# Optimization experiments

Measured on AMD Instinct MI355X. Metric: run time of the kernel, lower is better.

## Reference

```python
import jax, jax.numpy as jnp
import numpy as np

B, S, D = 8, 2048, 768
H, HD = 12, 64  # num_heads, head_dim = embed_dim // num_heads
EPS = 1e-6


def setup_inputs() -> dict:
    key = jax.random.key(0)
    ks = jax.random.split(key, 9)
    sc = 0.02
    return {
        "x": jax.random.normal(ks[0], (B, S, D), jnp.float32),
        "Wq": jax.random.normal(ks[1], (H, D, HD), jnp.float32) * sc,
        "bq": jax.random.normal(ks[2], (H, HD), jnp.float32) * sc,
        "Wk": jax.random.normal(ks[3], (H, D, HD), jnp.float32) * sc,
        "bk": jax.random.normal(ks[4], (H, HD), jnp.float32) * sc,
        "Wv": jax.random.normal(ks[5], (H, D, HD), jnp.float32) * sc,
        "bv": jax.random.normal(ks[6], (H, HD), jnp.float32) * sc,
        "Wp": jax.random.normal(ks[7], (D, D), jnp.float32) * sc,
        "bp": jax.random.normal(ks[8], (D,), jnp.float32) * sc,
    }


def reference(x, Wq, bq, Wk, bk, Wv, bv, Wp, bp):
    # Batched per-head projections (the torch loop over heads, vectorized).
    Q = jnp.einsum("bsd,hde->bhse", x, Wq) + bq[:, None, :]  # [B,H,S,HD]
    K = jnp.einsum("bsd,hde->bhse", x, Wk) + bk[:, None, :]
    V = jnp.einsum("bsd,hde->bhse", x, Wv) + bv[:, None, :]
    scale = jnp.sqrt(jnp.float32(HD)) + EPS  # intended 1/sqrt(head_dim) scaling
    scores = jnp.einsum("bhse,bhte->bhst", Q, K) / scale  # [B,H,S,S]
    attn = jax.nn.softmax(scores, axis=-1)
    ctx = jnp.einsum("bhst,bhte->bhse", attn, V)  # [B,H,S,HD]
    # concat heads along last dim (head i -> slice i*HD:(i+1)*HD), then project
    ctx = jnp.transpose(ctx, (0, 2, 1, 3)).reshape(B, S, H * HD)
    return ctx @ Wp + bp
```

## Files before the change

kernel.cpp:

```cpp
#include <hip/hip_runtime.h>
#include <hip/hip_bf16.h>
#include <stdint.h>

#define B_  8
#define S_  2048
#define D_  768
#define H_  12
#define HD_ 64
#define BH_ (B_*H_)
#define M_  (B_*S_)

typedef __bf16 bf16;
typedef __bf16 bf16x8 __attribute__((ext_vector_type(8)));
typedef __bf16 bf16x4 __attribute__((ext_vector_type(4)));
typedef short  short4v __attribute__((ext_vector_type(4)));
typedef float  f32x4  __attribute__((ext_vector_type(4)));

#define QSCALE2 0.18033685756901243f

#if __has_builtin(__builtin_amdgcn_exp2f)
#define EXP2(x) __builtin_amdgcn_exp2f(x)
#else
#define EXP2(x) exp2f(x)
#endif

#define LDS_BARRIER() asm volatile("s_waitcnt lgkmcnt(0)\n\ts_barrier" ::: "memory")

#define GLD16(gptr, lptr) __builtin_amdgcn_global_load_lds( \
    (const __attribute__((address_space(1))) uint32_t*)(gptr), \
    (__attribute__((address_space(3))) uint32_t*)(lptr), 16, 0, 0)

#if __has_builtin(__builtin_amdgcn_mfma_f32_16x16x16bf16_1k)
static __device__ inline f32x4 mfma16(bf16x4 a, bf16x4 b, f32x4 c) {
  return __builtin_amdgcn_mfma_f32_16x16x16bf16_1k(
      __builtin_bit_cast(short4v, a), __builtin_bit_cast(short4v, b), c, 0, 0, 0);
}
#else
static __device__ inline f32x4 mfma16(bf16x4 a, bf16x4 b, f32x4 c) {
  bf16 z = (bf16)0.f;
  bf16x8 a8 = {a[0], a[1], a[2], a[3], z, z, z, z};
  bf16x8 b8 = {b[0], b[1], b[2], b[3], z, z, z, z};
  return __builtin_amdgcn_mfma_f32_16x16x32_bf16(a8, b8, c, 0, 0, 0);
}
#endif

__global__ __launch_bounds__(256) void f2b(const float* __restrict__ src,
                                           bf16* __restrict__ dst, int n) {
  int i = (blockIdx.x * 256 + threadIdx.x) * 8;
  if (i >= n) return;
  float4 a = *(const float4*)(src + i);
  float4 b = *(const float4*)(src + i + 4);
  bf16 o[8] = {(bf16)a.x, (bf16)a.y, (bf16)a.z, (bf16)a.w,
               (bf16)b.x, (bf16)b.y, (bf16)b.z, (bf16)b.w};
  *(uint4*)(dst + i) = *(const uint4*)o;
}

__global__ __launch_bounds__(256) void transpose64_f2b(const float* __restrict__ src,
                                                       bf16* __restrict__ dst,
                                                       int R, int C) {
  __shared__ bf16 t[64][72];
  int mat = blockIdx.z;
  const float* s = src + (size_t)mat * R * C;
  bf16* d = dst + (size_t)mat * C * R;
  int r0 = blockIdx.x * 64, c0 = blockIdx.y * 64;
  int tid = threadIdx.x;
  #pragma unroll
  for (int it = 0; it < 4; ++it) {
    int i = (tid >> 4) + it * 16;
    int j = (tid & 15) * 4;
    float4 v = *(const float4*)(s + (size_t)(r0 + i) * C + c0 + j);
    t[j + 0][i] = (bf16)v.x; t[j + 1][i] = (bf16)v.y;
    t[j + 2][i] = (bf16)v.z; t[j + 3][i] = (bf16)v.w;
  }
  __syncthreads();
  #pragma unroll
  for (int it = 0; it < 4; ++it) {
    int i = (tid >> 4) + it * 16;
    int j = (tid & 15) * 4;
    bf16* p = d + (size_t)(c0 + i) * R + r0 + j;
    p[0] = t[i][j]; p[1] = t[i][j + 1]; p[2] = t[i][j + 2]; p[3] = t[i][j + 3];
  }
}

__global__ __launch_bounds__(256) void prep_w(
    const float* __restrict__ Wq, const float* __restrict__ Wk,
    const float* __restrict__ Wv, const float* __restrict__ bq,
    const float* __restrict__ bk, const float* __restrict__ bv,
    bf16* __restrict__ Wt, float* __restrict__ ball)
{
  int z = blockIdx.z;
  int tid = threadIdx.x;
  if (z == 36) {
    int i = blockIdx.x * 256 + tid;
    if (i < 2304) {
      float v = (i < 768) ? bq[i] : (i < 1536 ? bk[i - 768] : bv[i - 1536]);
      ball[i] = v;
    }
    return;
  }
  __shared__ bf16 t[64][72];
  int w = z / 12, h = z % 12;
  const float* s = (w == 0 ? Wq : (w == 1 ? Wk : Wv)) + (size_t)h * 768 * 64;
  bf16* d = Wt + (size_t)z * 64 * 768;
  int r0 = blockIdx.x * 64;
  #pragma unroll
  for (int it = 0; it < 4; ++it) {
    int i = (tid >> 4) + it * 16;
    int j = (tid & 15) * 4;
    float4 v = *(const float4*)(s + (size_t)(r0 + i) * 64 + j);
    t[j + 0][i] = (bf16)v.x; t[j + 1][i] = (bf16)v.y;
    t[j + 2][i] = (bf16)v.z; t[j + 3][i] = (bf16)v.w;
  }
  __syncthreads();
  #pragma unroll
  for (int it = 0; it < 4; ++it) {
    int i = (tid >> 4) + it * 16;
    int j = (tid & 15) * 4;
    bf16* p = d + (size_t)i * 768 + r0 + j;
    p[0] = t[i][j]; p[1] = t[i][j + 1]; p[2] = t[i][j + 2]; p[3] = t[i][j + 3];
  }
}

template <int MODE>
__global__ __launch_bounds__(256, 3) void gemm_bt(
    const bf16* __restrict__ A, const bf16* __restrict__ Bt,
    const float* __restrict__ bias, float* __restrict__ C,
    bf16* __restrict__ Qo, bf16* __restrict__ Ko, bf16* __restrict__ Vo,
    int Mdim, int Ndim, int Kdim)
{
  __shared__ bf16 smem[16384];
  int tid = threadIdx.x;
  int wave = tid >> 6, lane = tid & 63;
  int wm = wave & 1, wn = wave >> 1;
  int m0 = blockIdx.x * 128, n0 = blockIdx.y * 128;
  int lm = lane & 15, lq = lane >> 4;

  int c0_ = wave * 2;
  int r_in = lane >> 2;
  int ps   = lane & 3;
  int rowA0 = c0_ * 16 + r_in;
  int rowA1 = rowA0 + 16;
  int ls0 = ps ^ (rowA0 & 3);
  int ls1 = ps ^ (rowA1 & 3);

  f32x4 zero = {0.f, 0.f, 0.f, 0.f};
  f32x4 acc[4][4];
  #pragma unroll
  for (int i = 0; i < 4; ++i)
    #pragma unroll
    for (int j = 0; j < 4; ++j) acc[i][j] = zero;

  int NK = Kdim >> 5;

  GLD16(A  + (size_t)(m0 + rowA0) * Kdim + ls0 * 8, &smem[c0_ * 512]);
  GLD16(A  + (size_t)(m0 + rowA1) * Kdim + ls1 * 8, &smem[c0_ * 512 + 512]);
  GLD16(Bt + (size_t)(n0 + rowA0) * Kdim + ls0 * 8, &smem[4096 + c0_ * 512]);
  GLD16(Bt + (size_t)(n0 + rowA1) * Kdim + ls1 * 8, &smem[4096 + c0_ * 512 + 512]);
  __syncthreads();

  for (int kk = 0; kk < NK; ++kk) {
    int cb = (kk & 1) << 13;
    int nb = 8192 - cb;

    if (kk + 1 < NK) {
      int k0 = (kk + 1) * 32;
      GLD16(A  + (size_t)(m0 + rowA0) * Kdim + k0 + ls0 * 8, &smem[nb + c0_ * 512]);
      GLD16(A  + (size_t)(m0 + rowA1) * Kdim + k0 + ls1 * 8, &smem[nb + c0_ * 512 + 512]);
      GLD16(Bt + (size_t)(n0 + rowA0) * Kdim + k0 + ls0 * 8, &smem[nb + 4096 + c0_ * 512]);
      GLD16(Bt + (size_t)(n0 + rowA1) * Kdim + k0 + ls1 * 8, &smem[nb + 4096 + c0_ * 512 + 512]);
    }

    bf16x8 af[4], bfr[4];
    #pragma unroll
    for (int i = 0; i < 4; ++i) {
      int ra = wm * 64 + i * 16 + lm;
      af[i] = *(const bf16x8*)(&smem[cb + ra * 32 + ((lq ^ (ra & 3)) * 8)]);
    }
    #pragma unroll
    for (int j = 0; j < 4; ++j) {
      int rb = wn * 64 + j * 16 + lm;
      bfr[j] = *(const bf16x8*)(&smem[cb + 4096 + rb * 32 + ((lq ^ (rb & 3)) * 8)]);
    }
    __builtin_amdgcn_s_setprio(1);
    #pragma unroll
    for (int i = 0; i < 4; ++i)
      #pragma unroll
      for (int j = 0; j < 4; ++j)
        acc[i][j] = __builtin_amdgcn_mfma_f32_16x16x32_bf16(af[i], bfr[j], acc[i][j], 0, 0, 0);
    __builtin_amdgcn_s_setprio(0);

    asm volatile("s_waitcnt vmcnt(0)" ::: "memory");
    LDS_BARRIER();
  }

  int mbase = m0 + wm * 64, nbase = n0 + wn * 64;
  #pragma unroll
  for (int j = 0; j < 4; ++j) {
    int n = nbase + j * 16 + lm;
    float bv_ = bias[n];
    if (MODE == 0) {
      #pragma unroll
      for (int i = 0; i < 4; ++i)
        #pragma unroll
        for (int r = 0; r < 4; ++r) {
          int m = mbase + i * 16 + lq * 4 + r;
          C[(size_t)m * Ndim + n] = acc[i][j][r] + bv_;
        }
    } else {
      int which = n / 768;
      int rem = n - which * 768;
      int h = rem >> 6, e = rem & 63;
      float scl = (which == 0) ? QSCALE2 : 1.0f;
      if (which == 2) {
        #pragma unroll
        for (int i = 0; i < 4; ++i)
          #pragma unroll
          for (int r = 0; r < 4; ++r) {
            int m = mbase + i * 16 + lq * 4 + r;
            int b = m >> 11, s = m & 2047;
            Vo[((size_t)(b * H_ + h) * 64 + e) * S_ + s] = (bf16)(acc[i][j][r] + bv_);
          }
      } else {
        bf16* dst = (which == 0) ? Qo : Ko;
        #pragma unroll
        for (int i = 0; i < 4; ++i)
          #pragma unroll
          for (int r = 0; r < 4; ++r) {
            int m = mbase + i * 16 + lq * 4 + r;
            int b = m >> 11, s = m & 2047;
            dst[((size_t)(b * H_ + h) * S_ + s) * 64 + e] = (bf16)((acc[i][j][r] + bv_) * scl);
          }
      }
    }
  }
}

__global__ __launch_bounds__(256, 4) void flash_attn(
    const bf16* __restrict__ Q, const bf16* __restrict__ K,
    const bf16* __restrict__ Vt, bf16* __restrict__ ctx)
{
  __shared__ bf16 smem[16384];
  int tid = threadIdx.x;
  int wave = tid >> 6, lane = tid & 63;
  int lm = lane & 15, lq = lane >> 4;
  int x7 = lane & 7;

  int id = blockIdx.x;
  int xcd = id & 7, jj = id >> 3;
  int bh = xcd * 12 + (jj >> 4);
  int q0 = (jj & 15) * 128;

  const bf16* Qb = Q + (size_t)bh * S_ * 64;
  const bf16* Kb = K + (size_t)bh * S_ * 64;
  const bf16* Vb = Vt + (size_t)bh * 64 * S_;

  int rr = lane >> 3;
  int ls = (lane & 7) ^ rr;
  const bf16* gk0 = Kb + (size_t)(wave * 16 + rr) * 64 + ls * 8;
  const bf16* gv0 = Vb + (size_t)(wave * 16 + rr) * S_ + ls * 8;

  {
    const bf16* gq = Qb + (size_t)(q0 + wave * 32 + rr) * 64 + ls * 8;
    #pragma unroll
    for (int c = 0; c < 4; ++c)
      GLD16(gq + (size_t)c * 512, &smem[8192 + (wave * 4 + c) * 512]);
    GLD16(gk0,                    &smem[wave * 1024]);
    GLD16(gk0 + 512,              &smem[wave * 1024 + 512]);
    GLD16(gv0,                    &smem[4096 + wave * 1024]);
    GLD16(gv0 + (size_t)8 * S_,   &smem[4096 + wave * 1024 + 512]);
  }
  __syncthreads();

  int qw = wave * 32;
  bf16x8 qf[2][2];
  #pragma unroll
  for (int ks = 0; ks < 2; ++ks)
    #pragma unroll
    for (int mi = 0; mi < 2; ++mi)
      qf[ks][mi] = *(const bf16x8*)(&smem[8192 + (qw + mi * 16 + lm) * 64
                                          + ((ks * 4 + lq) ^ x7) * 8]);
  LDS_BARRIER();

  f32x4 zero = {0.f, 0.f, 0.f, 0.f};
  f32x4 O[2][4];
  float lsum[2] = {0.f, 0.f};
  #pragma unroll
  for (int i = 0; i < 2; ++i)
    #pragma unroll
    for (int d = 0; d < 4; ++d) O[i][d] = zero;

  for (int t = 0; t < 32; ++t) {
    int cb = (t & 1) << 13;
    int nb = 8192 - cb;

    if (t + 1 < 32) {
      const bf16* gk = gk0 + (size_t)(t + 1) * 4096;
      const bf16* gv = gv0 + (size_t)(t + 1) * 64;
      GLD16(gk,                   &smem[nb + wave * 1024]);
      GLD16(gk + 512,             &smem[nb + wave * 1024 + 512]);
      GLD16(gv,                   &smem[nb + 4096 + wave * 1024]);
      GLD16(gv + (size_t)8 * S_,  &smem[nb + 4096 + wave * 1024 + 512]);
    }

    f32x4 sacc[2][4];
    #pragma unroll
    for (int i = 0; i < 2; ++i)
      #pragma unroll
      for (int j = 0; j < 4; ++j) sacc[i][j] = zero;
    __builtin_amdgcn_s_setprio(1);
    #pragma unroll
    for (int ks = 0; ks < 2; ++ks) {
      #pragma unroll
      for (int ni = 0; ni < 4; ++ni) {
        bf16x8 ak = *(const bf16x8*)(&smem[cb + (ni * 16 + lm) * 64
                                           + ((ks * 4 + lq) ^ x7) * 8]);
        sacc[0][ni] = __builtin_amdgcn_mfma_f32_16x16x32_bf16(ak, qf[ks][0], sacc[0][ni], 0, 0, 0);
        sacc[1][ni] = __builtin_amdgcn_mfma_f32_16x16x32_bf16(ak, qf[ks][1], sacc[1][ni], 0, 0, 0);
      }
    }
    __builtin_amdgcn_s_setprio(0);

    bf16x4 pexp[2][4];
    #pragma unroll
    for (int mi = 0; mi < 2; ++mi) {
      #pragma unroll
      for (int ni = 0; ni < 4; ++ni) {
        float e0 = EXP2(sacc[mi][ni][0]);
        float e1 = EXP2(sacc[mi][ni][1]);
        float e2 = EXP2(sacc[mi][ni][2]);
        float e3 = EXP2(sacc[mi][ni][3]);
        lsum[mi] += (e0 + e1) + (e2 + e3);
        bf16x4 px = {(bf16)e0, (bf16)e1, (bf16)e2, (bf16)e3};
        pexp[mi][ni] = px;
      }
    }

    __builtin_amdgcn_s_setprio(1);
    #pragma unroll
    for (int ni = 0; ni < 4; ++ni) {
      #pragma unroll
      for (int dj = 0; dj < 4; ++dj) {
        bf16x4 vb = *(const bf16x4*)(&smem[cb + 4096 + (dj * 16 + lm) * 64
                                           + ((ni * 2 + (lq >> 1)) ^ x7) * 8
                                           + (lq & 1) * 4]);
        O[0][dj] = mfma16(pexp[0][ni], vb, O[0][dj]);
        O[1][dj] = mfma16(pexp[1][ni], vb, O[1][dj]);
      }
    }
    __builtin_amdgcn_s_setprio(0);

    asm volatile("s_waitcnt vmcnt(0)" ::: "memory");
    LDS_BARRIER();
  }

  float ls_[2];
  #pragma unroll
  for (int mi = 0; mi < 2; ++mi) {
    float rs = lsum[mi];
    rs += __shfl_xor(rs, 16);
    rs += __shfl_xor(rs, 32);
    ls_[mi] = rs;
  }

  int b = bh / H_, h = bh % H_;
  #pragma unroll
  for (int mi = 0; mi < 2; ++mi) {
    #pragma unroll
    for (int r = 0; r < 4; ++r) {
      int s = q0 + qw + mi * 16 + lq * 4 + r;
      float lv = __shfl(ls_[mi], lq * 4 + r);
      float linv = 1.0f / lv;
      #pragma unroll
      for (int dj = 0; dj < 4; ++dj) {
        int d = dj * 16 + lm;
        ctx[(size_t)(b * S_ + s) * D_ + h * 64 + d] = (bf16)(O[mi][dj][r] * linv);
      }
    }
  }
}

extern "C" void kernel_launch(void* const* d_in, const int* in_sizes, int n_in,
                              void* d_out, int out_size, void* d_ws, size_t ws_size,
                              hipStream_t stream)
{
  const float* x  = (const float*)d_in[0];
  const float* Wq = (const float*)d_in[1];
  const float* bq = (const float*)d_in[2];
  const float* Wk = (const float*)d_in[3];
  const float* bk = (const float*)d_in[4];
  const float* Wv = (const float*)d_in[5];
  const float* bv = (const float*)d_in[6];
  const float* Wp = (const float*)d_in[7];
  const float* bp = (const float*)d_in[8];
  float* out = (float*)d_out;

  char* w = (char*)d_ws;
  const size_t SZ  = (size_t)BH_ * S_ * 64;
  const size_t SZb = SZ * sizeof(bf16);
  bf16*  xb   = (bf16*)(w);
  bf16*  Qb   = (bf16*)(w + 1 * SZb);
  bf16*  Kb   = (bf16*)(w + 2 * SZb);
  bf16*  Vtb  = (bf16*)(w + 3 * SZb);
  bf16*  Wt   = (bf16*)(w + 4 * SZb);
  bf16*  Wpt  = Wt;
  float* ball = (float*)(w + 4 * SZb + 2304 * 768 * 2);
  bf16*  ctx  = xb;

  f2b<<<(int)(SZ / (256 * 8)), 256, 0, stream>>>(x, xb, (int)SZ);
  prep_w<<<dim3(12, 1, 37), 256, 0, stream>>>(Wq, Wk, Wv, bq, bk, bv, Wt, ball);

  gemm_bt<1><<<dim3(128, 18), 256, 0, stream>>>(xb, Wt, ball, (float*)nullptr,
                                                Qb, Kb, Vtb, M_, 2304, 768);
  transpose64_f2b<<<dim3(12, 12, 1), 256, 0, stream>>>(Wp, Wpt, 768, 768);
  flash_attn<<<1536, 256, 0, stream>>>(Qb, Kb, Vtb, ctx);
  gemm_bt<0><<<dim3(128, 6), 256, 0, stream>>>(ctx, Wpt, bp, out,
                                               (bf16*)nullptr, (bf16*)nullptr, (bf16*)nullptr,
                                               M_, 768, 768);
}
```

Measured before the change: 360.0 us.

## Triple-buffer GEMM LDS tiles with two-stage-ahead global prefetch

Changes the GEMM main loop from double to triple buffering in shared memory, issuing global-to-LDS loads two K-steps ahead and waiting with vmcnt(4) so one stage stays in flight. This aims to hide global load latency behind the MFMA work. LDS use rises from 32KB to 48KB per block, which may lower occupancy under the launch bounds of 3 blocks per CU.

```diff
diff --git a/kernel.cpp b/kernel.cpp
--- a/kernel.cpp
+++ b/kernel.cpp
@@ -128,7 +128,7 @@
     bf16* __restrict__ Qo, bf16* __restrict__ Ko, bf16* __restrict__ Vo,
     int Mdim, int Ndim, int Kdim)
 {
-  __shared__ bf16 smem[16384];
+  __shared__ bf16 smem[24576];
   int tid = threadIdx.x;
   int wave = tid >> 6, lane = tid & 63;
   int wm = wave & 1, wn = wave >> 1;
@@ -143,6 +143,11 @@
   int ls0 = ps ^ (rowA0 & 3);
   int ls1 = ps ^ (rowA1 & 3);
 
+  const bf16* gA0 = A  + (size_t)(m0 + rowA0) * Kdim + ls0 * 8;
+  const bf16* gA1 = A  + (size_t)(m0 + rowA1) * Kdim + ls1 * 8;
+  const bf16* gB0 = Bt + (size_t)(n0 + rowA0) * Kdim + ls0 * 8;
+  const bf16* gB1 = Bt + (size_t)(n0 + rowA1) * Kdim + ls1 * 8;
+
   f32x4 zero = {0.f, 0.f, 0.f, 0.f};
   f32x4 acc[4][4];
   #pragma unroll
@@ -152,34 +157,38 @@
 
   int NK = Kdim >> 5;
 
-  GLD16(A  + (size_t)(m0 + rowA0) * Kdim + ls0 * 8, &smem[c0_ * 512]);
-  GLD16(A  + (size_t)(m0 + rowA1) * Kdim + ls1 * 8, &smem[c0_ * 512 + 512]);
-  GLD16(Bt + (size_t)(n0 + rowA0) * Kdim + ls0 * 8, &smem[4096 + c0_ * 512]);
-  GLD16(Bt + (size_t)(n0 + rowA1) * Kdim + ls1 * 8, &smem[4096 + c0_ * 512 + 512]);
-  __syncthreads();
-
+  GLD16(gA0,      &smem[c0_ * 512]);
+  GLD16(gA1,      &smem[c0_ * 512 + 512]);
+  GLD16(gB0,      &smem[4096 + c0_ * 512]);
+  GLD16(gB1,      &smem[4096 + c0_ * 512 + 512]);
+  GLD16(gA0 + 32, &smem[8192 + c0_ * 512]);
+  GLD16(gA1 + 32, &smem[8192 + c0_ * 512 + 512]);
+  GLD16(gB0 + 32, &smem[8192 + 4096 + c0_ * 512]);
+  GLD16(gB1 + 32, &smem[8192 + 4096 + c0_ * 512 + 512]);
+  asm volatile("s_waitcnt vmcnt(4)" ::: "memory");
+  LDS_BARRIER();
+
+  int cur = 0;
   for (int kk = 0; kk < NK; ++kk) {
-    int cb = (kk & 1) << 13;
-    int nb = 8192 - cb;
-
-    if (kk + 1 < NK) {
-      int k0 = (kk + 1) * 32;
-      GLD16(A  + (size_t)(m0 + rowA0) * Kdim + k0 + ls0 * 8, &smem[nb + c0_ * 512]);
-      GLD16(A  + (size_t)(m0 + rowA1) * Kdim + k0 + ls1 * 8, &smem[nb + c0_ * 512 + 512]);
-      GLD16(Bt + (size_t)(n0 + rowA0) * Kdim + k0 + ls0 * 8, &smem[nb + 4096 + c0_ * 512]);
-      GLD16(Bt + (size_t)(n0 + rowA1) * Kdim + k0 + ls1 * 8, &smem[nb + 4096 + c0_ * 512 + 512]);
+    if (kk + 2 < NK) {
+      int pre = cur + 16384; if (pre >= 24576) pre -= 24576;
+      int k0 = (kk + 2) * 32;
+      GLD16(gA0 + k0, &smem[pre + c0_ * 512]);
+      GLD16(gA1 + k0, &smem[pre + c0_ * 512 + 512]);
+      GLD16(gB0 + k0, &smem[pre + 4096 + c0_ * 512]);
+      GLD16(gB1 + k0, &smem[pre + 4096 + c0_ * 512 + 512]);
     }
 
     bf16x8 af[4], bfr[4];
     #pragma unroll
     for (int i = 0; i < 4; ++i) {
       int ra = wm * 64 + i * 16 + lm;
-      af[i] = *(const bf16x8*)(&smem[cb + ra * 32 + ((lq ^ (ra & 3)) * 8)]);
+      af[i] = *(const bf16x8*)(&smem[cur + ra * 32 + ((lq ^ (ra & 3)) * 8)]);
     }
     #pragma unroll
     for (int j = 0; j < 4; ++j) {
       int rb = wn * 64 + j * 16 + lm;
-      bfr[j] = *(const bf16x8*)(&smem[cb + 4096 + rb * 32 + ((lq ^ (rb & 3)) * 8)]);
+      bfr[j] = *(const bf16x8*)(&smem[cur + 4096 + rb * 32 + ((lq ^ (rb & 3)) * 8)]);
     }
     __builtin_amdgcn_s_setprio(1);
     #pragma unroll
@@ -189,8 +198,11 @@
         acc[i][j] = __builtin_amdgcn_mfma_f32_16x16x32_bf16(af[i], bfr[j], acc[i][j], 0, 0, 0);
     __builtin_amdgcn_s_setprio(0);
 
-    asm volatile("s_waitcnt vmcnt(0)" ::: "memory");
+    if (kk + 2 < NK) { asm volatile("s_waitcnt vmcnt(4)" ::: "memory"); }
+    else             { asm volatile("s_waitcnt vmcnt(0)" ::: "memory"); }
     LDS_BARRIER();
+
+    cur += 8192; if (cur >= 24576) cur = 0;
   }
 
   int mbase = m0 + wm * 64, nbase = n0 + wn * 64;
```

Measured after the change: 355.8 us. About the same (-1.2%).
